# Kernel tuning notes

Hardware: AMD Instinct MI355X
Metric: run time of the kernel (lower is better)

Reference implementation:

```python
import jax, jax.numpy as jnp
import numpy as np

B, N, F, K = 8, 4096, 512, 100
EPS = 1e-15  # torch_geometric dense_mincut_pool EPS
BN_EPS = 1e-5


def setup_inputs() -> dict:
    key = jax.random.key(0)
    k1, k2, k3 = jax.random.split(key, 3)
    x_nodes = jax.random.normal(k1, (B, N, F), jnp.float32)
    adj_matrix = jax.random.uniform(k2, (B, N, N), jnp.float32)  # dense weighted adjacency
    x_masks = jnp.ones((B, N), dtype=bool)
    W = jax.random.normal(k3, (K, F), jnp.float32) / np.float32(np.sqrt(F))  # nn.Linear weight
    b = jnp.zeros((K,), jnp.float32)
    gamma = jnp.ones((K,), jnp.float32)   # BatchNorm1d weight
    beta = jnp.zeros((K,), jnp.float32)   # BatchNorm1d bias
    return {"x_nodes": x_nodes, "adj_matrix": adj_matrix, "x_masks": x_masks,
            "W": W, "b": b, "gamma": gamma, "beta": beta}


def reference(x_nodes, adj_matrix, x_masks, W, b, gamma, beta):
    # s = self.mlp(x_nodes[:, :, :in_features])
    x = x_nodes[:, :, :F]                       # [B,N,F]
    s = jnp.einsum('bnf,kf->bnk', x, W) + b     # [B,N,K]

    # --- dense_mincut_pool (torch_geometric) ---
    m = x_masks[..., None].astype(x.dtype)      # [B,N,1]
    s = jax.nn.softmax(s, axis=-1) * m
    x = x * m

    out = jnp.einsum('bnk,bnf->bkf', s, x)      # s^T x  [B,K,F]
    As = jnp.matmul(adj_matrix, s)              # A s    [B,N,K]
    out_adj = jnp.einsum('bnk,bnl->bkl', s, As) # s^T A s [B,K,K]

    # mincut loss: -Tr(s^T A s) / Tr(s^T D s)
    mincut_num = jnp.trace(out_adj, axis1=1, axis2=2)          # [B]
    deg = adj_matrix.sum(-1)                                    # [B,N]
    mincut_den = jnp.einsum('bn,bnk,bnk->b', deg, s, s)         # Tr(s^T D s)
    mc = jnp.mean(-(mincut_num / mincut_den))

    # orthogonality loss: || ss/||ss||_F - I/sqrt(K) ||_F
    ss = jnp.einsum('bnk,bnl->bkl', s, s)                       # [B,K,K]
    ss_fro = jnp.sqrt(jnp.sum(ss * ss, axis=(1, 2), keepdims=True))
    i_s = jnp.eye(K, dtype=x.dtype) / jnp.sqrt(jnp.asarray(K, x.dtype))
    o = jnp.mean(jnp.sqrt(jnp.sum((ss / ss_fro - i_s) ** 2, axis=(1, 2))))

    # zero diagonal then symmetric degree-normalize coarsened adjacency
    eye = jnp.eye(K, dtype=x.dtype)
    out_adj = out_adj * (1.0 - eye)
    d = jnp.sqrt(out_adj.sum(-1))[:, None, :] + EPS             # [B,1,K]
    out_adj = out_adj / d / jnp.swapaxes(d, 1, 2)

    # BatchNorm1d(K) on [B,K,F] (training mode, biased variance), then squeeze(1) (no-op, K>1)
    mean = out.mean(axis=(0, 2), keepdims=True)
    var = out.var(axis=(0, 2), keepdims=True)
    x_af_pool = gamma[None, :, None] * (out - mean) / jnp.sqrt(var + BN_EPS) + beta[None, :, None]

    return x_af_pool, out_adj, mc + o
```

## Files before the change

kernel.cpp:

```cpp
#include <hip/hip_runtime.h>
#include <stdint.h>

#define BB 8
#define NN 4096
#define FF 512
#define KK 100
#define K2 112

typedef __attribute__((ext_vector_type(8))) short short8;
typedef __attribute__((ext_vector_type(4))) float f32x4;

__device__ __forceinline__ unsigned short f2b(float f){
  unsigned u = __float_as_uint(f);
  return (unsigned short)((u + 0x7FFFu + ((u >> 16) & 1u)) >> 16);
}

__device__ __forceinline__ f32x4 mfma16(short8 a, short8 b, f32x4 c){
  return __builtin_amdgcn_mfma_f32_16x16x32_bf16(a, b, c, 0, 0, 0);
}

__global__ void k0_wconv(const float* __restrict__ W, unsigned short* __restrict__ Wb){
  int i = blockIdx.x * 256 + threadIdx.x;
  if (i >= K2 * FF) return;
  int k = i >> 9;
  Wb[i] = (k < KK) ? f2b(W[i]) : (unsigned short)0;
}

__launch_bounds__(256)
__global__ void k1_logits(const float* __restrict__ x, const float* __restrict__ bias,
                          const unsigned short* __restrict__ Wb,
                          unsigned short* __restrict__ sT, unsigned short* __restrict__ xT,
                          float* __restrict__ ssum){
  __shared__ unsigned short xtile[64 * 40];
  __shared__ unsigned short slds[112 * 72];
  const int t = threadIdx.x, bx = blockIdx.x;
  const int b = bx >> 6, n0 = (bx & 63) << 6;
  const int w = t >> 6, ln15 = t & 15, g = (t & 63) >> 4;
  const float* xb = x + ((size_t)b * NN + n0) * FF;
  const int r = t >> 2, c0 = (t & 3) << 3;
  f32x4 acc[7];
  #pragma unroll
  for (int i = 0; i < 7; ++i) acc[i] = (f32x4){0.f, 0.f, 0.f, 0.f};

  #pragma unroll 1
  for (int fs = 0; fs < 16; ++fs){
    const int f0 = fs << 5;
    const float4* src = (const float4*)(xb + (size_t)r * FF + f0 + c0);
    float4 a0 = src[0], a1 = src[1];
    uint4 pk;
    pk.x = (unsigned)f2b(a0.x) | ((unsigned)f2b(a0.y) << 16);
    pk.y = (unsigned)f2b(a0.z) | ((unsigned)f2b(a0.w) << 16);
    pk.z = (unsigned)f2b(a1.x) | ((unsigned)f2b(a1.y) << 16);
    pk.w = (unsigned)f2b(a1.z) | ((unsigned)f2b(a1.w) << 16);
    *(uint4*)&xtile[r * 40 + c0] = pk;
    __syncthreads();
    short8 av = *(const short8*)&xtile[(16 * w + ln15) * 40 + 8 * g];
    #pragma unroll
    for (int kf = 0; kf < 7; ++kf){
      short8 bv = *(const short8*)(Wb + (size_t)(16 * kf + ln15) * FF + f0 + 8 * g);
      acc[kf] = mfma16(av, bv, acc[kf]);
    }
    {
      const int fi = t >> 3, nc = t & 7;
      uint4 o;
      o.x = (unsigned)xtile[(8*nc+0)*40+fi] | ((unsigned)xtile[(8*nc+1)*40+fi] << 16);
      o.y = (unsigned)xtile[(8*nc+2)*40+fi] | ((unsigned)xtile[(8*nc+3)*40+fi] << 16);
      o.z = (unsigned)xtile[(8*nc+4)*40+fi] | ((unsigned)xtile[(8*nc+5)*40+fi] << 16);
      o.w = (unsigned)xtile[(8*nc+6)*40+fi] | ((unsigned)xtile[(8*nc+7)*40+fi] << 16);
      *(uint4*)(xT + ((size_t)b * FF + f0 + fi) * NN + n0 + 8 * nc) = o;
    }
    __syncthreads();
  }

  #pragma unroll
  for (int rr = 0; rr < 4; ++rr){
    const int nloc = 16 * w + 4 * g + rr;
    float lg[7];
    float m = -1e30f;
    #pragma unroll
    for (int kf = 0; kf < 7; ++kf){
      int k = 16 * kf + ln15;
      float v = (k < KK) ? (acc[kf][rr] + bias[k]) : -1e30f;
      lg[kf] = v; m = fmaxf(m, v);
    }
    #pragma unroll
    for (int d = 1; d < 16; d <<= 1) m = fmaxf(m, __shfl_xor(m, d, 16));
    float sum = 0.f, sq = 0.f;
    float ev[7];
    #pragma unroll
    for (int kf = 0; kf < 7; ++kf){
      int k = 16 * kf + ln15;
      float e = (k < KK) ? __expf(lg[kf] - m) : 0.f;
      ev[kf] = e; sum += e; sq += e * e;
    }
    #pragma unroll
    for (int d = 1; d < 16; d <<= 1){ sum += __shfl_xor(sum, d, 16); sq += __shfl_xor(sq, d, 16); }
    float inv = 1.f / sum;
    #pragma unroll
    for (int kf = 0; kf < 7; ++kf)
      slds[(16 * kf + ln15) * 72 + nloc] = f2b(ev[kf] * inv);
    if (ln15 == 0) ssum[b * NN + n0 + nloc] = sq * inv * inv;
  }
  __syncthreads();
  for (int c = t; c < 112 * 8; c += 256){
    int row = c >> 3, nc = c & 7;
    uint4 v = *(const uint4*)&slds[row * 72 + 8 * nc];
    *(uint4*)(sT + ((size_t)b * K2 + row) * NN + n0 + 8 * nc) = v;
  }
}

__launch_bounds__(256)
__global__ void k2_adj(const float* __restrict__ adj, const unsigned short* __restrict__ sT,
                       unsigned short* __restrict__ AsT, float* __restrict__ deg){
  __shared__ unsigned short atile[64 * 40];
  __shared__ unsigned short stile[112 * 40];
  const int t = threadIdx.x, bx = blockIdx.x;
  const int b = bx >> 6, n0 = (bx & 63) << 6;
  const int w = t >> 6, ln15 = t & 15, g = (t & 63) >> 4;
  const float* ab = adj + ((size_t)b * NN + n0) * NN;
  const unsigned short* sb = sT + (size_t)b * K2 * NN;
  const int r = t >> 2, c0 = (t & 3) << 3;
  f32x4 acc[7];
  #pragma unroll
  for (int i = 0; i < 7; ++i) acc[i] = (f32x4){0.f, 0.f, 0.f, 0.f};
  float dacc = 0.f;
  float4 a0, a1;
  uint4 sv0 = {0,0,0,0}, sv1 = {0,0,0,0}, sv2 = {0,0,0,0}, sv3 = {0,0,0,0};
  {
    const float4* ap = (const float4*)(ab + (size_t)r * NN + c0);
    a0 = ap[0]; a1 = ap[1];
  }
  if (t < 112){
    const uint4* sp = (const uint4*)(sb + (size_t)t * NN);
    sv0 = sp[0]; sv1 = sp[1]; sv2 = sp[2]; sv3 = sp[3];
  }
  #pragma unroll 1
  for (int it = 0; it < 128; ++it){
    dacc += a0.x + a0.y + a0.z + a0.w + a1.x + a1.y + a1.z + a1.w;
    uint4 pk;
    pk.x = (unsigned)f2b(a0.x) | ((unsigned)f2b(a0.y) << 16);
    pk.y = (unsigned)f2b(a0.z) | ((unsigned)f2b(a0.w) << 16);
    pk.z = (unsigned)f2b(a1.x) | ((unsigned)f2b(a1.y) << 16);
    pk.w = (unsigned)f2b(a1.z) | ((unsigned)f2b(a1.w) << 16);
    *(uint4*)&atile[r * 40 + c0] = pk;
    if (t < 112){
      uint4* sd = (uint4*)&stile[t * 40];
      sd[0] = sv0; sd[1] = sv1; sd[2] = sv2; sd[3] = sv3;
    }
    __syncthreads();
    if (it + 1 < 128){
      const float4* ap = (const float4*)(ab + (size_t)r * NN + (it + 1) * 32 + c0);
      a0 = ap[0]; a1 = ap[1];
      if (t < 112){
        const uint4* sp = (const uint4*)(sb + (size_t)t * NN + (it + 1) * 32);
        sv0 = sp[0]; sv1 = sp[1]; sv2 = sp[2]; sv3 = sp[3];
      }
    }
    short8 av = *(const short8*)&atile[(16 * w + ln15) * 40 + 8 * g];
    #pragma unroll
    for (int kf = 0; kf < 7; ++kf){
      short8 bv = *(const short8*)&stile[(16 * kf + ln15) * 40 + 8 * g];
      acc[kf] = mfma16(av, bv, acc[kf]);
    }
    __syncthreads();
  }
  dacc += __shfl_xor(dacc, 1);
  dacc += __shfl_xor(dacc, 2);
  if ((t & 3) == 0) deg[b * NN + n0 + r] = dacc;
  #pragma unroll
  for (int kf = 0; kf < 7; ++kf){
    int k = 16 * kf + ln15;
    uint2 ov;
    ov.x = (unsigned)f2b(acc[kf][0]) | ((unsigned)f2b(acc[kf][1]) << 16);
    ov.y = (unsigned)f2b(acc[kf][2]) | ((unsigned)f2b(acc[kf][3]) << 16);
    *(uint2*)(AsT + ((size_t)b * K2 + k) * NN + n0 + 16 * w + 4 * g) = ov;
  }
}

__launch_bounds__(256)
__global__ void k3_out_kernel(const unsigned short* __restrict__ sT,
                              const unsigned short* __restrict__ xT,
                              float* __restrict__ outraw){
  const int t = threadIdx.x, bx = blockIdx.x;
  const int b = bx >> 4, ft = (bx >> 2) & 3, nc = bx & 3;
  const int w = t >> 6, ln15 = t & 15, g = (t & 63) >> 4;
  const unsigned short* Ab = sT + (size_t)b * K2 * NN;
  const unsigned short* Bb = xT + ((size_t)b * FF + ft * 128 + 32 * w) * NN;
  f32x4 acc[7][2];
  #pragma unroll
  for (int i = 0; i < 7; ++i){ acc[i][0] = (f32x4){0,0,0,0}; acc[i][1] = (f32x4){0,0,0,0}; }
  const int base = nc * 1024 + 8 * g;
  #pragma unroll 1
  for (int s = 0; s < 32; ++s){
    const int l0 = base + s * 32;
    short8 bv0 = *(const short8*)(Bb + (size_t)ln15 * NN + l0);
    short8 bv1 = *(const short8*)(Bb + (size_t)(16 + ln15) * NN + l0);
    #pragma unroll
    for (int mf = 0; mf < 7; ++mf){
      short8 av = *(const short8*)(Ab + (size_t)(16 * mf + ln15) * NN + l0);
      acc[mf][0] = mfma16(av, bv0, acc[mf][0]);
      acc[mf][1] = mfma16(av, bv1, acc[mf][1]);
    }
  }
  const int f0 = ft * 128 + 32 * w;
  #pragma unroll
  for (int mf = 0; mf < 7; ++mf)
    #pragma unroll
    for (int i = 0; i < 2; ++i)
      #pragma unroll
      for (int rr = 0; rr < 4; ++rr){
        int k = 16 * mf + 4 * g + rr;
        atomicAdd(&outraw[((size_t)b * K2 + k) * FF + f0 + 16 * i + ln15], acc[mf][i][rr]);
      }
}

__launch_bounds__(256)
__global__ void k3_kk_kernel(const unsigned short* __restrict__ A,
                             const unsigned short* __restrict__ Bt,
                             float* __restrict__ Cacc){
  const int t = threadIdx.x, bx = blockIdx.x;
  const int b = bx >> 3, nc = bx & 7;
  const int w = t >> 6, ln15 = t & 15, g = (t & 63) >> 4;
  const unsigned short* Ab = A + (size_t)b * K2 * NN;
  const unsigned short* Bb = Bt + (size_t)b * K2 * NN;
  const int nf0 = 2 * w;
  const int nf1 = (2 * w + 1 < 7) ? 2 * w + 1 : 0;
  f32x4 acc[7][2];
  #pragma unroll
  for (int i = 0; i < 7; ++i){ acc[i][0] = (f32x4){0,0,0,0}; acc[i][1] = (f32x4){0,0,0,0}; }
  const int base = nc * 512 + 8 * g;
  #pragma unroll 1
  for (int s = 0; s < 16; ++s){
    const int l0 = base + s * 32;
    short8 bv0 = *(const short8*)(Bb + (size_t)(16 * nf0 + ln15) * NN + l0);
    short8 bv1 = *(const short8*)(Bb + (size_t)(16 * nf1 + ln15) * NN + l0);
    #pragma unroll
    for (int mf = 0; mf < 7; ++mf){
      short8 av = *(const short8*)(Ab + (size_t)(16 * mf + ln15) * NN + l0);
      acc[mf][0] = mfma16(av, bv0, acc[mf][0]);
      acc[mf][1] = mfma16(av, bv1, acc[mf][1]);
    }
  }
  #pragma unroll
  for (int mf = 0; mf < 7; ++mf)
    #pragma unroll
    for (int rr = 0; rr < 4; ++rr){
      int k = 16 * mf + 4 * g + rr;
      atomicAdd(&Cacc[((size_t)b * K2 + k) * K2 + 16 * nf0 + ln15], acc[mf][0][rr]);
      if (2 * w + 1 < 7)
        atomicAdd(&Cacc[((size_t)b * K2 + k) * K2 + 16 * nf1 + ln15], acc[mf][1][rr]);
    }
}

__global__ void k4a_kernel(const float* __restrict__ deg, const float* __restrict__ ssum,
                           const float* __restrict__ oadj, float* __restrict__ nums,
                           float* __restrict__ dens){
  __shared__ float red[256];
  const int b = blockIdx.x, t = threadIdx.x;
  float p = 0.f;
  for (int n = t; n < NN; n += 256) p += deg[b * NN + n] * ssum[b * NN + n];
  red[t] = p; __syncthreads();
  for (int s = 128; s > 0; s >>= 1){ if (t < s) red[t] += red[t + s]; __syncthreads(); }
  if (t == 0) dens[b] = red[0];
  __syncthreads();
  float q = (t < KK) ? oadj[((size_t)b * K2 + t) * K2 + t] : 0.f;
  red[t] = q; __syncthreads();
  for (int s = 128; s > 0; s >>= 1){ if (t < s) red[t] += red[t + s]; __syncthreads(); }
  if (t == 0) nums[b] = red[0];
}

__global__ void k4b_kernel(const float* __restrict__ outraw, const float* __restrict__ gamma,
                           const float* __restrict__ beta, float* __restrict__ dout){
  __shared__ float r1[256], r2[256];
  const int k = blockIdx.x, t = threadIdx.x;
  float s1 = 0.f, s2v = 0.f;
  for (int j = t; j < BB * FF; j += 256){
    int b = j >> 9, f = j & (FF - 1);
    float v = outraw[((size_t)b * K2 + k) * FF + f];
    s1 += v; s2v += v * v;
  }
  r1[t] = s1; r2[t] = s2v; __syncthreads();
  for (int s = 128; s > 0; s >>= 1){
    if (t < s){ r1[t] += r1[t + s]; r2[t] += r2[t + s]; }
    __syncthreads();
  }
  const float mean = r1[0] * (1.f / (BB * FF));
  const float var = r2[0] * (1.f / (BB * FF)) - mean * mean;
  const float sc = gamma[k] * rsqrtf(var + 1e-5f);
  const float sh = beta[k] - mean * sc;
  for (int j = t; j < BB * FF; j += 256){
    int b = j >> 9, f = j & (FF - 1);
    float v = outraw[((size_t)b * K2 + k) * FF + f];
    dout[((size_t)b * KK + k) * FF + f] = v * sc + sh;
  }
}

__global__ void k4c_kernel(const float* __restrict__ oadj, const float* __restrict__ ssr,
                           float* __restrict__ dout, float* __restrict__ obuf){
  __shared__ float dvals[KK];
  __shared__ float red[256];
  const int b = blockIdx.x, t = threadIdx.x;
  const float* oa = oadj + (size_t)b * K2 * K2;
  const float* sr = ssr + (size_t)b * K2 * K2;
  if (t < KK){
    float s = 0.f;
    for (int l = 0; l < KK; ++l) if (l != t) s += oa[t * K2 + l];
    dvals[t] = sqrtf(s) + 1e-15f;
  }
  float p = 0.f;
  for (int e = t; e < KK * KK; e += 256){
    int k = e / KK, l = e - k * KK;
    float v = sr[k * K2 + l];
    p += v * v;
  }
  red[t] = p; __syncthreads();
  for (int s = 128; s > 0; s >>= 1){ if (t < s) red[t] += red[t + s]; __syncthreads(); }
  const float inv = 1.f / sqrtf(red[0]);
  __syncthreads();
  float q = 0.f;
  for (int e = t; e < KK * KK; e += 256){
    int k = e / KK, l = e - k * KK;
    float ov = (k == l) ? 0.f : oa[k * K2 + l];
    dout[409600 + (size_t)b * KK * KK + e] = ov / (dvals[k] * dvals[l]);
    float sv = sr[k * K2 + l] * inv - ((k == l) ? 0.1f : 0.f);
    q += sv * sv;
  }
  red[t] = q; __syncthreads();
  for (int s = 128; s > 0; s >>= 1){ if (t < s) red[t] += red[t + s]; __syncthreads(); }
  if (t == 0) obuf[b] = sqrtf(red[0]);
}

__global__ void k4d_kernel(const float* __restrict__ nums, const float* __restrict__ dens,
                           const float* __restrict__ obuf, float* __restrict__ dout){
  if (threadIdx.x == 0){
    float mc = 0.f, o = 0.f;
    for (int b = 0; b < BB; ++b){ mc += -nums[b] / dens[b]; o += obuf[b]; }
    dout[489600] = mc * (1.f / BB) + o * (1.f / BB);
  }
}

extern "C" void kernel_launch(void* const* d_in, const int* in_sizes, int n_in,
                              void* d_out, int out_size, void* d_ws, size_t ws_size,
                              hipStream_t stream){
  const float* x     = (const float*)d_in[0];
  const float* adj   = (const float*)d_in[1];
  const float* W     = (const float*)d_in[3];
  const float* bias  = (const float*)d_in[4];
  const float* gamma = (const float*)d_in[5];
  const float* beta  = (const float*)d_in[6];
  float* out = (float*)d_out;
  char* ws = (char*)d_ws;

  unsigned short* sT  = (unsigned short*)(ws + 0);
  unsigned short* xT  = (unsigned short*)(ws + 7340032);
  unsigned short* AsT = (unsigned short*)(ws + 40894464);
  float* deg    = (float*)(ws + 48234496);
  float* ssum   = (float*)(ws + 48365568);
  float* outraw = (float*)(ws + 48496640);
  float* oadj   = (float*)(ws + 50331648);
  float* ssr    = (float*)(ws + 50733056);
  unsigned short* Wb = (unsigned short*)(ws + 51134464);
  float* nums   = (float*)(ws + 51249152);
  float* dens   = nums + 8;
  float* obuf   = nums + 16;

  hipMemsetAsync(outraw, 0, 2637824, stream);

  k0_wconv<<<224, 256, 0, stream>>>(W, Wb);
  k1_logits<<<512, 256, 0, stream>>>(x, bias, Wb, sT, xT, ssum);
  k2_adj<<<512, 256, 0, stream>>>(adj, sT, AsT, deg);
  k3_out_kernel<<<128, 256, 0, stream>>>(sT, xT, outraw);
  k3_kk_kernel<<<64, 256, 0, stream>>>(sT, AsT, oadj);
  k3_kk_kernel<<<64, 256, 0, stream>>>(sT, sT, ssr);
  k4a_kernel<<<8, 256, 0, stream>>>(deg, ssum, oadj, nums, dens);
  k4b_kernel<<<100, 256, 0, stream>>>(outraw, gamma, beta, out);
  k4c_kernel<<<8, 256, 0, stream>>>(oadj, ssr, out, obuf);
  k4d_kernel<<<1, 64, 0, stream>>>(nums, dens, obuf, out);
}
```

Measured before the change: 367.2 us.

## Drop LDS staging in adj GEMM, replace atomics with split-K partials, fuse tail kernels

Measured after the change: 579.7 us. +57.9%, slower.

```diff
diff --git a/kernel.cpp b/kernel.cpp
--- a/kernel.cpp
+++ b/kernel.cpp
@@ -10,6 +10,8 @@
 typedef __attribute__((ext_vector_type(8))) short short8;
 typedef __attribute__((ext_vector_type(4))) float f32x4;
 
+union CV8 { uint4 u; short8 s; };
+
 __device__ __forceinline__ unsigned short f2b(float f){
   unsigned u = __float_as_uint(f);
   return (unsigned short)((u + 0x7FFFu + ((u >> 16) & 1u)) >> 16);
@@ -19,8 +21,10 @@
   return __builtin_amdgcn_mfma_f32_16x16x32_bf16(a, b, c, 0, 0, 0);
 }
 
-__global__ void k0_wconv(const float* __restrict__ W, unsigned short* __restrict__ Wb){
+__global__ void k0_wconv(const float* __restrict__ W, unsigned short* __restrict__ Wb,
+                         float* __restrict__ dout){
   int i = blockIdx.x * 256 + threadIdx.x;
+  if (i == 0) dout[489600] = 0.f;
   if (i >= K2 * FF) return;
   int k = i >> 9;
   Wb[i] = (k < KK) ? f2b(W[i]) : (unsigned short)0;
@@ -34,7 +38,7 @@
   __shared__ unsigned short xtile[64 * 40];
   __shared__ unsigned short slds[112 * 72];
   const int t = threadIdx.x, bx = blockIdx.x;
-  const int b = bx >> 6, n0 = (bx & 63) << 6;
+  const int b = bx & 7, n0 = ((bx >> 3) & 63) << 6;
   const int w = t >> 6, ln15 = t & 15, g = (t & 63) >> 4;
   const float* xb = x + ((size_t)b * NN + n0) * FF;
   const int r = t >> 2, c0 = (t & 3) << 3;
@@ -112,61 +116,46 @@
 __launch_bounds__(256)
 __global__ void k2_adj(const float* __restrict__ adj, const unsigned short* __restrict__ sT,
                        unsigned short* __restrict__ AsT, float* __restrict__ deg){
-  __shared__ unsigned short atile[64 * 40];
-  __shared__ unsigned short stile[112 * 40];
   const int t = threadIdx.x, bx = blockIdx.x;
-  const int b = bx >> 6, n0 = (bx & 63) << 6;
+  const int b = bx & 7, n0 = (bx >> 3) << 6;
   const int w = t >> 6, ln15 = t & 15, g = (t & 63) >> 4;
-  const float* ab = adj + ((size_t)b * NN + n0) * NN;
-  const unsigned short* sb = sT + (size_t)b * K2 * NN;
-  const int r = t >> 2, c0 = (t & 3) << 3;
+  const int row = n0 + 16 * w + ln15;
+  const float* ap = adj + ((size_t)b * NN + row) * NN + 8 * g;
+  const unsigned short* sp = sT + ((size_t)b * K2 + ln15) * NN + 8 * g;
   f32x4 acc[7];
   #pragma unroll
   for (int i = 0; i < 7; ++i) acc[i] = (f32x4){0.f, 0.f, 0.f, 0.f};
   float dacc = 0.f;
-  float4 a0, a1;
-  uint4 sv0 = {0,0,0,0}, sv1 = {0,0,0,0}, sv2 = {0,0,0,0}, sv3 = {0,0,0,0};
-  {
-    const float4* ap = (const float4*)(ab + (size_t)r * NN + c0);
-    a0 = ap[0]; a1 = ap[1];
-  }
-  if (t < 112){
-    const uint4* sp = (const uint4*)(sb + (size_t)t * NN);
-    sv0 = sp[0]; sv1 = sp[1]; sv2 = sp[2]; sv3 = sp[3];
-  }
+  float4 a0 = *(const float4*)(ap), a1 = *(const float4*)(ap + 4);
+  short8 bv[7];
+  #pragma unroll
+  for (int kf = 0; kf < 7; ++kf) bv[kf] = *(const short8*)(sp + (size_t)(16 * kf) * NN);
   #pragma unroll 1
   for (int it = 0; it < 128; ++it){
+    const int itn = (it + 1 < 128) ? it + 1 : 127;
+    const float* ap2 = ap + itn * 32;
+    float4 na0 = *(const float4*)(ap2), na1 = *(const float4*)(ap2 + 4);
+    short8 nbv[7];
+    #pragma unroll
+    for (int kf = 0; kf < 7; ++kf)
+      nbv[kf] = *(const short8*)(sp + (size_t)(16 * kf) * NN + itn * 32);
     dacc += a0.x + a0.y + a0.z + a0.w + a1.x + a1.y + a1.z + a1.w;
     uint4 pk;
     pk.x = (unsigned)f2b(a0.x) | ((unsigned)f2b(a0.y) << 16);
     pk.y = (unsigned)f2b(a0.z) | ((unsigned)f2b(a0.w) << 16);
     pk.z = (unsigned)f2b(a1.x) | ((unsigned)f2b(a1.y) << 16);
     pk.w = (unsigned)f2b(a1.z) | ((unsigned)f2b(a1.w) << 16);
-    *(uint4*)&atile[r * 40 + c0] = pk;
-    if (t < 112){
-      uint4* sd = (uint4*)&stile[t * 40];
-      sd[0] = sv0; sd[1] = sv1; sd[2] = sv2; sd[3] = sv3;
-    }
-    __syncthreads();
-    if (it + 1 < 128){
-      const float4* ap = (const float4*)(ab + (size_t)r * NN + (it + 1) * 32 + c0);
-      a0 = ap[0]; a1 = ap[1];
-      if (t < 112){
-        const uint4* sp = (const uint4*)(sb + (size_t)t * NN + (it + 1) * 32);
-        sv0 = sp[0]; sv1 = sp[1]; sv2 = sp[2]; sv3 = sp[3];
-      }
-    }
-    short8 av = *(const short8*)&atile[(16 * w + ln15) * 40 + 8 * g];
-    #pragma unroll
-    for (int kf = 0; kf < 7; ++kf){
-      short8 bv = *(const short8*)&stile[(16 * kf + ln15) * 40 + 8 * g];
-      acc[kf] = mfma16(av, bv, acc[kf]);
-    }
-    __syncthreads();
-  }
-  dacc += __shfl_xor(dacc, 1);
-  dacc += __shfl_xor(dacc, 2);
-  if ((t & 3) == 0) deg[b * NN + n0 + r] = dacc;
+    CV8 cv; cv.u = pk;
+    short8 av = cv.s;
+    #pragma unroll
+    for (int kf = 0; kf < 7; ++kf) acc[kf] = mfma16(av, bv[kf], acc[kf]);
+    a0 = na0; a1 = na1;
+    #pragma unroll
+    for (int kf = 0; kf < 7; ++kf) bv[kf] = nbv[kf];
+  }
+  dacc += __shfl_xor(dacc, 16);
+  dacc += __shfl_xor(dacc, 32);
+  if ((t & 63) < 16) deg[b * NN + row] = dacc;
   #pragma unroll
   for (int kf = 0; kf < 7; ++kf){
     int k = 16 * kf + ln15;
@@ -180,51 +169,12 @@
 __launch_bounds__(256)
 __global__ void k3_out_kernel(const unsigned short* __restrict__ sT,
                               const unsigned short* __restrict__ xT,
-                              float* __restrict__ outraw){
+                              float* __restrict__ outp){
   const int t = threadIdx.x, bx = blockIdx.x;
-  const int b = bx >> 4, ft = (bx >> 2) & 3, nc = bx & 3;
+  const int b = bx & 7, ft = (bx >> 3) & 3, nc = bx >> 5;
   const int w = t >> 6, ln15 = t & 15, g = (t & 63) >> 4;
   const unsigned short* Ab = sT + (size_t)b * K2 * NN;
   const unsigned short* Bb = xT + ((size_t)b * FF + ft * 128 + 32 * w) * NN;
-  f32x4 acc[7][2];
-  #pragma unroll
-  for (int i = 0; i < 7; ++i){ acc[i][0] = (f32x4){0,0,0,0}; acc[i][1] = (f32x4){0,0,0,0}; }
-  const int base = nc * 1024 + 8 * g;
-  #pragma unroll 1
-  for (int s = 0; s < 32; ++s){
-    const int l0 = base + s * 32;
-    short8 bv0 = *(const short8*)(Bb + (size_t)ln15 * NN + l0);
-    short8 bv1 = *(const short8*)(Bb + (size_t)(16 + ln15) * NN + l0);
-    #pragma unroll
-    for (int mf = 0; mf < 7; ++mf){
-      short8 av = *(const short8*)(Ab + (size_t)(16 * mf + ln15) * NN + l0);
-      acc[mf][0] = mfma16(av, bv0, acc[mf][0]);
-      acc[mf][1] = mfma16(av, bv1, acc[mf][1]);
-    }
-  }
-  const int f0 = ft * 128 + 32 * w;
-  #pragma unroll
-  for (int mf = 0; mf < 7; ++mf)
-    #pragma unroll
-    for (int i = 0; i < 2; ++i)
-      #pragma unroll
-      for (int rr = 0; rr < 4; ++rr){
-        int k = 16 * mf + 4 * g + rr;
-        atomicAdd(&outraw[((size_t)b * K2 + k) * FF + f0 + 16 * i + ln15], acc[mf][i][rr]);
-      }
-}
-
-__launch_bounds__(256)
-__global__ void k3_kk_kernel(const unsigned short* __restrict__ A,
-                             const unsigned short* __restrict__ Bt,
-                             float* __restrict__ Cacc){
-  const int t = threadIdx.x, bx = blockIdx.x;
-  const int b = bx >> 3, nc = bx & 7;
-  const int w = t >> 6, ln15 = t & 15, g = (t & 63) >> 4;
-  const unsigned short* Ab = A + (size_t)b * K2 * NN;
-  const unsigned short* Bb = Bt + (size_t)b * K2 * NN;
-  const int nf0 = 2 * w;
-  const int nf1 = (2 * w + 1 < 7) ? 2 * w + 1 : 0;
   f32x4 acc[7][2];
   #pragma unroll
   for (int i = 0; i < 7; ++i){ acc[i][0] = (f32x4){0,0,0,0}; acc[i][1] = (f32x4){0,0,0,0}; }
@@ -232,8 +182,8 @@
   #pragma unroll 1
   for (int s = 0; s < 16; ++s){
     const int l0 = base + s * 32;
-    short8 bv0 = *(const short8*)(Bb + (size_t)(16 * nf0 + ln15) * NN + l0);
-    short8 bv1 = *(const short8*)(Bb + (size_t)(16 * nf1 + ln15) * NN + l0);
+    short8 bv0 = *(const short8*)(Bb + (size_t)ln15 * NN + l0);
+    short8 bv1 = *(const short8*)(Bb + (size_t)(16 + ln15) * NN + l0);
     #pragma unroll
     for (int mf = 0; mf < 7; ++mf){
       short8 av = *(const short8*)(Ab + (size_t)(16 * mf + ln15) * NN + l0);
@@ -241,43 +191,90 @@
       acc[mf][1] = mfma16(av, bv1, acc[mf][1]);
     }
   }
+  const int f0 = ft * 128 + 32 * w;
+  float* ob = outp + ((size_t)nc * BB + b) * (K2 * FF);
+  #pragma unroll
+  for (int mf = 0; mf < 7; ++mf)
+    #pragma unroll
+    for (int i = 0; i < 2; ++i)
+      #pragma unroll
+      for (int rr = 0; rr < 4; ++rr){
+        int k = 16 * mf + 4 * g + rr;
+        ob[(size_t)k * FF + f0 + 16 * i + ln15] = acc[mf][i][rr];
+      }
+}
+
+__launch_bounds__(256)
+__global__ void k3_kk_kernel(const unsigned short* __restrict__ sT,
+                             const unsigned short* __restrict__ AsT,
+                             float* __restrict__ kkp){
+  const int t = threadIdx.x, bx = blockIdx.x;
+  const int b = bx & 7, nc = (bx >> 3) & 15, mat = bx >> 7;
+  const unsigned short* Ab = sT + (size_t)b * K2 * NN;
+  const unsigned short* Bb = (mat ? sT : AsT) + (size_t)b * K2 * NN;
+  const int w = t >> 6, ln15 = t & 15, g = (t & 63) >> 4;
+  const int nf0 = 2 * w;
+  const int nf1 = (2 * w + 1 < 7) ? 2 * w + 1 : 0;
+  f32x4 acc[7][2];
+  #pragma unroll
+  for (int i = 0; i < 7; ++i){ acc[i][0] = (f32x4){0,0,0,0}; acc[i][1] = (f32x4){0,0,0,0}; }
+  const int base = nc * 256 + 8 * g;
+  #pragma unroll 1
+  for (int s = 0; s < 8; ++s){
+    const int l0 = base + s * 32;
+    short8 bv0 = *(const short8*)(Bb + (size_t)(16 * nf0 + ln15) * NN + l0);
+    short8 bv1 = *(const short8*)(Bb + (size_t)(16 * nf1 + ln15) * NN + l0);
+    #pragma unroll
+    for (int mf = 0; mf < 7; ++mf){
+      short8 av = *(const short8*)(Ab + (size_t)(16 * mf + ln15) * NN + l0);
+      acc[mf][0] = mfma16(av, bv0, acc[mf][0]);
+      acc[mf][1] = mfma16(av, bv1, acc[mf][1]);
+    }
+  }
+  float* ob = kkp + ((size_t)(mat * 16 + nc) * BB + b) * (K2 * K2);
   #pragma unroll
   for (int mf = 0; mf < 7; ++mf)
     #pragma unroll
     for (int rr = 0; rr < 4; ++rr){
       int k = 16 * mf + 4 * g + rr;
-      atomicAdd(&Cacc[((size_t)b * K2 + k) * K2 + 16 * nf0 + ln15], acc[mf][0][rr]);
+      ob[(size_t)k * K2 + 16 * nf0 + ln15] = acc[mf][0][rr];
       if (2 * w + 1 < 7)
-        atomicAdd(&Cacc[((size_t)b * K2 + k) * K2 + 16 * nf1 + ln15], acc[mf][1][rr]);
+        ob[(size_t)k * K2 + 16 * nf1 + ln15] = acc[mf][1][rr];
     }
 }
 
 __global__ void k4a_kernel(const float* __restrict__ deg, const float* __restrict__ ssum,
-                           const float* __restrict__ oadj, float* __restrict__ nums,
-                           float* __restrict__ dens){
-  __shared__ float red[256];
+                           const float* __restrict__ kkp, float* __restrict__ dout){
+  __shared__ float r1[256], r2[256];
   const int b = blockIdx.x, t = threadIdx.x;
   float p = 0.f;
   for (int n = t; n < NN; n += 256) p += deg[b * NN + n] * ssum[b * NN + n];
-  red[t] = p; __syncthreads();
-  for (int s = 128; s > 0; s >>= 1){ if (t < s) red[t] += red[t + s]; __syncthreads(); }
-  if (t == 0) dens[b] = red[0];
-  __syncthreads();
-  float q = (t < KK) ? oadj[((size_t)b * K2 + t) * K2 + t] : 0.f;
-  red[t] = q; __syncthreads();
-  for (int s = 128; s > 0; s >>= 1){ if (t < s) red[t] += red[t + s]; __syncthreads(); }
-  if (t == 0) nums[b] = red[0];
-}
-
-__global__ void k4b_kernel(const float* __restrict__ outraw, const float* __restrict__ gamma,
+  float q = 0.f;
+  for (int e = t; e < 16 * KK; e += 256){
+    int nc = e / KK, k = e - nc * KK;
+    q += kkp[((size_t)nc * BB + b) * (K2 * K2) + (size_t)k * K2 + k];
+  }
+  r1[t] = p; r2[t] = q; __syncthreads();
+  for (int s = 128; s > 0; s >>= 1){
+    if (t < s){ r1[t] += r1[t + s]; r2[t] += r2[t + s]; }
+    __syncthreads();
+  }
+  if (t == 0) atomicAdd(&dout[489600], -(r2[0] / r1[0]) * 0.125f);
+}
+
+__global__ void k4b_kernel(const float* __restrict__ outp, const float* __restrict__ gamma,
                            const float* __restrict__ beta, float* __restrict__ dout){
+  __shared__ float vbuf[BB * FF];
   __shared__ float r1[256], r2[256];
   const int k = blockIdx.x, t = threadIdx.x;
   float s1 = 0.f, s2v = 0.f;
   for (int j = t; j < BB * FF; j += 256){
     int b = j >> 9, f = j & (FF - 1);
-    float v = outraw[((size_t)b * K2 + k) * FF + f];
-    s1 += v; s2v += v * v;
+    float v = 0.f;
+    #pragma unroll
+    for (int nc = 0; nc < 8; ++nc)
+      v += outp[((size_t)nc * BB + b) * (K2 * FF) + (size_t)k * FF + f];
+    vbuf[j] = v; s1 += v; s2v += v * v;
   }
   r1[t] = s1; r2[t] = s2v; __syncthreads();
   for (int s = 128; s > 0; s >>= 1){
@@ -290,29 +287,34 @@
   const float sh = beta[k] - mean * sc;
   for (int j = t; j < BB * FF; j += 256){
     int b = j >> 9, f = j & (FF - 1);
-    float v = outraw[((size_t)b * K2 + k) * FF + f];
-    dout[((size_t)b * KK + k) * FF + f] = v * sc + sh;
-  }
-}
-
-__global__ void k4c_kernel(const float* __restrict__ oadj, const float* __restrict__ ssr,
-                           float* __restrict__ dout, float* __restrict__ obuf){
+    dout[((size_t)b * KK + k) * FF + f] = vbuf[j] * sc + sh;
+  }
+}
+
+__global__ void k4c_kernel(const float* __restrict__ kkp, float* __restrict__ dout){
+  __shared__ float oa[KK * KK];
+  __shared__ float sr[KK * KK];
   __shared__ float dvals[KK];
   __shared__ float red[256];
   const int b = blockIdx.x, t = threadIdx.x;
-  const float* oa = oadj + (size_t)b * K2 * K2;
-  const float* sr = ssr + (size_t)b * K2 * K2;
+  for (int e = t; e < KK * KK; e += 256){
+    int k = e / KK, l = e - k * KK;
+    float so = 0.f, ss = 0.f;
+    #pragma unroll
+    for (int nc = 0; nc < 16; ++nc){
+      so += kkp[((size_t)nc * BB + b) * (K2 * K2) + (size_t)k * K2 + l];
+      ss += kkp[((size_t)(16 + nc) * BB + b) * (K2 * K2) + (size_t)k * K2 + l];
+    }
+    oa[e] = so; sr[e] = ss;
+  }
+  __syncthreads();
   if (t < KK){
     float s = 0.f;
-    for (int l = 0; l < KK; ++l) if (l != t) s += oa[t * K2 + l];
+    for (int l = 0; l < KK; ++l) if (l != t) s += oa[t * KK + l];
     dvals[t] = sqrtf(s) + 1e-15f;
   }
   float p = 0.f;
-  for (int e = t; e < KK * KK; e += 256){
-    int k = e / KK, l = e - k * KK;
-    float v = sr[k * K2 + l];
-    p += v * v;
-  }
+  for (int e = t; e < KK * KK; e += 256) p += sr[e] * sr[e];
   red[t] = p; __syncthreads();
   for (int s = 128; s > 0; s >>= 1){ if (t < s) red[t] += red[t + s]; __syncthreads(); }
   const float inv = 1.f / sqrtf(red[0]);
@@ -320,23 +322,14 @@
   float q = 0.f;
   for (int e = t; e < KK * KK; e += 256){
     int k = e / KK, l = e - k * KK;
-    float ov = (k == l) ? 0.f : oa[k * K2 + l];
+    float ov = (k == l) ? 0.f : oa[e];
     dout[409600 + (size_t)b * KK * KK + e] = ov / (dvals[k] * dvals[l]);
-    float sv = sr[k * K2 + l] * inv - ((k == l) ? 0.1f : 0.f);
+    float sv = sr[e] * inv - ((k == l) ? 0.1f : 0.f);
     q += sv * sv;
   }
   red[t] = q; __syncthreads();
   for (int s = 128; s > 0; s >>= 1){ if (t < s) red[t] += red[t + s]; __syncthreads(); }
-  if (t == 0) obuf[b] = sqrtf(red[0]);
-}
-
-__global__ void k4d_kernel(const float* __restrict__ nums, const float* __restrict__ dens,
-                           const float* __restrict__ obuf, float* __restrict__ dout){
-  if (threadIdx.x == 0){
-    float mc = 0.f, o = 0.f;
-    for (int b = 0; b < BB; ++b){ mc += -nums[b] / dens[b]; o += obuf[b]; }
-    dout[489600] = mc * (1.f / BB) + o * (1.f / BB);
-  }
+  if (t == 0) atomicAdd(&dout[489600], sqrtf(red[0]) * 0.125f);
 }
 
 extern "C" void kernel_launch(void* const* d_in, const int* in_sizes, int n_in,
@@ -356,24 +349,16 @@
   unsigned short* AsT = (unsigned short*)(ws + 40894464);
   float* deg    = (float*)(ws + 48234496);
   float* ssum   = (float*)(ws + 48365568);
-  float* outraw = (float*)(ws + 48496640);
-  float* oadj   = (float*)(ws + 50331648);
-  float* ssr    = (float*)(ws + 50733056);
-  unsigned short* Wb = (unsigned short*)(ws + 51134464);
-  float* nums   = (float*)(ws + 51249152);
-  float* dens   = nums + 8;
-  float* obuf   = nums + 16;
-
-  hipMemsetAsync(outraw, 0, 2637824, stream);
-
-  k0_wconv<<<224, 256, 0, stream>>>(W, Wb);
+  float* outp   = (float*)(ws + 48496640);
+  float* kkp    = (float*)(ws + 63176704);
+  unsigned short* Wb = (unsigned short*)(ws + 76021760);
+
+  k0_wconv<<<224, 256, 0, stream>>>(W, Wb, out);
   k1_logits<<<512, 256, 0, stream>>>(x, bias, Wb, sT, xT, ssum);
   k2_adj<<<512, 256, 0, stream>>>(adj, sT, AsT, deg);
-  k3_out_kernel<<<128, 256, 0, stream>>>(sT, xT, outraw);
-  k3_kk_kernel<<<64, 256, 0, stream>>>(sT, AsT, oadj);
-  k3_kk_kernel<<<64, 256, 0, stream>>>(sT, sT, ssr);
-  k4a_kernel<<<8, 256, 0, stream>>>(deg, ssum, oadj, nums, dens);
-  k4b_kernel<<<100, 256, 0, stream>>>(outraw, gamma, beta, out);
-  k4c_kernel<<<8, 256, 0, stream>>>(oadj, ssr, out, obuf);
-  k4d_kernel<<<1, 64, 0, stream>>>(nums, dens, obuf, out);
-}
+  k3_out_kernel<<<256, 256, 0, stream>>>(sT, xT, outp);
+  k3_kk_kernel<<<256, 256, 0, stream>>>(sT, AsT, kkp);
+  k4a_kernel<<<8, 256, 0, stream>>>(deg, ssum, kkp, out);
+  k4b_kernel<<<100, 256, 0, stream>>>(outp, gamma, beta, out);
+  k4c_kernel<<<8, 256, 0, stream>>>(kkp, out);
+}
```
